# Kernel optimization log

Hardware: AMD Instinct MI355X
Metric: run time of the kernel (lower is better)

## Reference

```python
import math
import jax, jax.numpy as jnp
import numpy as np

N = 50000      # nodes
E = 800000     # edges
H = 128        # hidden_dim
NR = 16        # num_radial
CUTOFF = 5.0
LN_EPS = 1e-5


def _ln(h, g, b):
    m = jnp.mean(h, axis=-1, keepdims=True)
    v = jnp.mean((h - m) ** 2, axis=-1, keepdims=True)
    return (h - m) * jax.lax.rsqrt(v + LN_EPS) * g + b


def _legendre(angle):
    # degree=4 -> 4 polynomial features
    c = jnp.cos(angle)
    p0 = jnp.ones_like(c)
    p1 = c
    p2 = (3.0 * c * p1 - 1.0 * p0) / 2.0
    p3 = (5.0 * c * p2 - 2.0 * p1) / 3.0
    return jnp.concatenate([p0, p1, p2, p3], axis=-1)


def setup_inputs() -> dict:
    key = jax.random.key(0)
    ks = jax.random.split(key, 16)
    ED = 2 * H + NR + 3  # edge feature dim = 275

    def w(k, shape, fan_in):
        return jax.random.normal(k, shape, jnp.float32) / np.sqrt(fan_in).astype(np.float32)

    return {
        "x": jax.random.normal(ks[0], (N, H), jnp.float32),
        "pos": jax.random.normal(ks[1], (N, 3), jnp.float32),
        "charge": jax.random.normal(ks[2], (N, 1), jnp.float32),
        "edge_attr": jax.random.uniform(ks[3], (E, 4), jnp.float32),
        "edge_index": jax.random.randint(ks[4], (2, E), 0, N),
        "We1": w(ks[5], (ED, H), ED), "be1": jnp.zeros((H,), jnp.float32),
        "g1": jnp.ones((H,), jnp.float32), "bt1": jnp.zeros((H,), jnp.float32),
        "We2": w(ks[6], (H, H), H), "be2": jnp.zeros((H,), jnp.float32),
        "Wn": w(ks[7], (2 * H, H), 2 * H), "bn": jnp.zeros((H,), jnp.float32),
        "gn": jnp.ones((H,), jnp.float32), "btn": jnp.zeros((H,), jnp.float32),
        "Wc1": w(ks[8], (H, H // 2), H), "bc1": jnp.zeros((H // 2,), jnp.float32),
        "Wc2": w(ks[9], (H // 2, 1), H // 2), "bc2": jnp.zeros((1,), jnp.float32),
    }


def reference(x, pos, charge, edge_attr, edge_index,
              We1, be1, g1, bt1, We2, be2, Wn, bn, gn, btn,
              Wc1, bc1, Wc2, bc2):
    src, dst = edge_index[0], edge_index[1]

    rel = pos[dst] - pos[src]                                   # [E,3]
    dist = jnp.sqrt(jnp.sum(rel ** 2, axis=-1, keepdims=True) + 1e-8)
    unit = rel / jnp.clip(dist, 1e-6)

    # edge-attribute gate via Legendre basis of angle/dihedral
    af = _legendre(edge_attr[:, 0:1])
    df = _legendre(edge_attr[:, 1:2])
    a_score = jnp.mean(jnp.abs(af), axis=-1, keepdims=True) * edge_attr[:, 2:3]
    d_score = jnp.mean(jnp.abs(df), axis=-1, keepdims=True) * edge_attr[:, 3:4]
    gate = jnp.clip(1.0 + 0.6 * (a_score + d_score), 0.35, 2.5)  # [E,1]

    # spherical Bessel radial basis
    freq = jnp.arange(1, NR + 1, dtype=jnp.float32) * (math.pi / CUTOFF)
    clipped = jnp.clip(dist, 1e-6)
    rad = jnp.sin(freq * clipped) / clipped                      # [E,NR]

    qs, qd = charge[src], charge[dst]
    ef = jnp.concatenate([
        x[src], x[dst], rad * gate, dist / CUTOFF * gate,
        qs * qd * gate, jnp.abs(qs - qd) * gate], axis=-1)       # [E,275]

    h = jax.nn.silu(ef @ We1 + be1)
    h = _ln(h, g1, bt1)
    eh = jax.nn.silu(h @ We2 + be2)                              # [E,H]

    ones = jnp.ones((eh.shape[0], 1), eh.dtype)
    cnt = jnp.clip(jax.ops.segment_sum(ones, src, num_segments=N), 1.0)
    agg = jax.ops.segment_sum(eh, src, num_segments=N) / cnt     # scatter-mean

    coord = jax.nn.silu(eh @ Wc1 + bc1) @ Wc2 + bc2              # [E,1]
    delta = jax.ops.segment_sum(unit * coord * gate, src, num_segments=N) / cnt

    x_new = x + _ln(jax.nn.silu(jnp.concatenate([x, agg], axis=-1) @ Wn + bn), gn, btn)
    pos_new = pos + 0.1 * delta
    return (x_new, pos_new)
```

## Files before the change

### kernel.cpp

```cpp
#include <hip/hip_runtime.h>
#include <hip/hip_bf16.h>
#include <math.h>


#define HDIM 128
#define GN   16
#define TILE 64
#define HS   136
#define AUXS 32
#define NS   264

#define B_BE1 0
#define B_G1  128
#define B_BT1 256
#define B_BE2 384
#define B_BC1 512
#define B_WC2 576
#define B_BC2 640
#define B_BN  704
#define B_GN  832
#define B_BTN 960
#define BIAS_N 1088

typedef unsigned int uint32;
typedef float f32x4 __attribute__((ext_vector_type(4)));
typedef float f32x2 __attribute__((ext_vector_type(2)));
typedef short short8 __attribute__((ext_vector_type(8)));
typedef unsigned short u16x4 __attribute__((ext_vector_type(4)));

__device__ __forceinline__ float bf2f(__hip_bfloat16 h) { return __bfloat162float(h); }

template<bool BF> __device__ __forceinline__ f32x2 ld2(const void* p, size_t i) {
  if constexpr (BF) {
    uint32 u; __builtin_memcpy(&u, (const char*)p + i * 2, 4);
    f32x2 r; r.x = __uint_as_float(u << 16); r.y = __uint_as_float(u & 0xffff0000u);
    return r;
  } else {
    f32x2 r; __builtin_memcpy(&r, (const char*)p + i * 4, 8);
    return r;
  }
}
template<bool BF> __device__ __forceinline__ float ld1(const void* p, size_t i) {
  if constexpr (BF) {
    __hip_bfloat16 h; __builtin_memcpy(&h, (const char*)p + i * 2, 2);
    return bf2f(h);
  } else {
    float v; __builtin_memcpy(&v, (const char*)p + i * 4, 4);
    return v;
  }
}
template<bool BF> __device__ __forceinline__ void st1(void* p, size_t i, float v) {
  if constexpr (BF) {
    __hip_bfloat16 h = __float2bfloat16(v);
    __builtin_memcpy((char*)p + i * 2, &h, 2);
  } else {
    __builtin_memcpy((char*)p + i * 4, &v, 4);
  }
}

__device__ __forceinline__ unsigned short f2bf(float v) {
  __hip_bfloat16 h = __float2bfloat16(v);
  unsigned short u; __builtin_memcpy(&u, &h, 2);
  return u;
}

template<bool BF> __device__ __forceinline__ short8 ldxrow(const void* x, int row, int col) {
  if constexpr (BF) {
    return *reinterpret_cast<const short8*>((const char*)x + ((size_t)row * HDIM + col) * 2);
  } else {
    const float* p = (const float*)x + (size_t)row * HDIM + col;
    f32x4 v0 = *reinterpret_cast<const f32x4*>(p);
    f32x4 v1 = *reinterpret_cast<const f32x4*>(p + 4);
    short8 a;
    a[0] = (short)f2bf(v0.x); a[1] = (short)f2bf(v0.y);
    a[2] = (short)f2bf(v0.z); a[3] = (short)f2bf(v0.w);
    a[4] = (short)f2bf(v1.x); a[5] = (short)f2bf(v1.y);
    a[6] = (short)f2bf(v1.z); a[7] = (short)f2bf(v1.w);
    return a;
  }
}

__device__ __forceinline__ float silu(float v) { return v / (1.0f + __expf(-v)); }

__device__ __forceinline__ f32x4 splat4(float v) {
  f32x4 r; r.x = v; r.y = v; r.z = v; r.w = v; return r;
}

__device__ __forceinline__ void wave_sync() {
  asm volatile("s_waitcnt lgkmcnt(0)" ::: "memory");
}

__global__ void probe_kernel(const uint32* g1, int* flag) {
  if (threadIdx.x == 0 && blockIdx.x == 0) *flag = (g1[0] == 0x3F800000u) ? 0 : 1;
}

__global__ void hist_kernel(const int* __restrict__ ei, int* __restrict__ cnt, int E) {
  int e = blockIdx.x * 256 + threadIdx.x;
  if (e < E) atomicAdd(&cnt[ei[e]], 1);
}

__global__ void __launch_bounds__(1024) scan_kernel(const int* __restrict__ cnt,
                                                    int* __restrict__ off, int N) {
  __shared__ int part[16];
  __shared__ int carry_s;
  const int t = threadIdx.x;
  const int wid = t >> 6, ln = t & 63;
  if (t == 0) carry_s = 0;
  __syncthreads();
  for (int base = 0; base < N; base += 1024) {
    const int v = (base + t < N) ? cnt[base + t] : 0;
    int inc = v;
#pragma unroll
    for (int s = 1; s < 64; s <<= 1) {
      int u = __shfl_up(inc, s);
      if (ln >= s) inc += u;
    }
    if (ln == 63) part[wid] = inc;
    __syncthreads();
    if (wid == 0) {
      int p = (ln < 16) ? part[ln] : 0;
#pragma unroll
      for (int s = 1; s < 16; s <<= 1) {
        int u = __shfl_up(p, s);
        if (ln >= s) p += u;
      }
      if (ln < 16) part[ln] = p;
    }
    __syncthreads();
    const int woff = (wid > 0) ? part[wid - 1] : 0;
    const int carry = carry_s;
    if (base + t < N) off[base + t] = carry + inc + woff - v;
    __syncthreads();
    if (t == 1023) carry_s = carry + part[15];
    __syncthreads();
  }
  if (t == 0) off[N] = carry_s;
}

__global__ void fill_kernel(const int* __restrict__ ei, const int* __restrict__ off,
                            int* __restrict__ cursor, int* __restrict__ eidx, int E) {
  int e = blockIdx.x * 256 + threadIdx.x;
  if (e < E) {
    int s = ei[e];
    int p = atomicAdd(&cursor[s], 1);
    eidx[off[s] + p] = e;
  }
}

template<bool BF>
__global__ void __launch_bounds__(256) prep_kernel(
    const void* __restrict__ pos, const void* __restrict__ charge,
    const void* __restrict__ We1, const void* __restrict__ We2,
    const void* __restrict__ Wc1, const void* __restrict__ Wn,
    const void* __restrict__ be1, const void* __restrict__ g1,
    const void* __restrict__ bt1, const void* __restrict__ be2,
    const void* __restrict__ bc1, const void* __restrict__ wc2,
    const void* __restrict__ bc2, const void* __restrict__ bn,
    const void* __restrict__ gn, const void* __restrict__ btn,
    const int* __restrict__ flag,
    float* __restrict__ posf, float* __restrict__ chgf, float* __restrict__ biasf,
    __hip_bfloat16* __restrict__ WT1, __hip_bfloat16* __restrict__ WT2,
    __hip_bfloat16* __restrict__ WTc1, __hip_bfloat16* __restrict__ WTn,
    int N) {
  if (*flag != (BF ? 1 : 0)) return;
  const int gt = blockIdx.x * 256 + threadIdx.x;
  const int gs = gridDim.x * 256;
  for (int i = gt; i < N * 3; i += gs) posf[i] = ld1<BF>(pos, i);
  for (int i = gt; i < N; i += gs) chgf[i] = ld1<BF>(charge, i);
  for (int i = gt; i < 128; i += gs) {
    biasf[B_BE1 + i] = ld1<BF>(be1, i);
    biasf[B_G1  + i] = ld1<BF>(g1, i);
    biasf[B_BT1 + i] = ld1<BF>(bt1, i);
    biasf[B_BE2 + i] = ld1<BF>(be2, i);
    biasf[B_BN  + i] = ld1<BF>(bn, i);
    biasf[B_GN  + i] = ld1<BF>(gn, i);
    biasf[B_BTN + i] = ld1<BF>(btn, i);
  }
  for (int i = gt; i < 64; i += gs) {
    biasf[B_BC1 + i] = ld1<BF>(bc1, i);
    biasf[B_WC2 + i] = ld1<BF>(wc2, i);
  }
  if (gt == 0) biasf[B_BC2] = ld1<BF>(bc2, 0);
  for (int i = gt; i < 128 * 288; i += gs) {
    int n = i / 288, k = i % 288;
    float v = (k < 275) ? ld1<BF>(We1, (size_t)k * 128 + n) : 0.f;
    WT1[i] = __float2bfloat16(v);
  }
  for (int i = gt; i < 128 * 128; i += gs) {
    int n = i / 128, k = i % 128;
    WT2[i] = __float2bfloat16(ld1<BF>(We2, (size_t)k * 128 + n));
  }
  for (int i = gt; i < 64 * 128; i += gs) {
    int n = i / 128, k = i % 128;
    WTc1[i] = __float2bfloat16(ld1<BF>(Wc1, (size_t)k * 64 + n));
  }
  for (int i = gt; i < 128 * 256; i += gs) {
    int n = i / 256, k = i % 256;
    WTn[i] = __float2bfloat16(ld1<BF>(Wn, (size_t)k * 128 + n));
  }
}

template<bool BF>
__global__ void __launch_bounds__(256, 2) edge_mfma_kernel(
    const void* __restrict__ x, const void* __restrict__ eattr,
    const int* __restrict__ ei,
    const int* __restrict__ off, const int* __restrict__ eidx,
    const int* __restrict__ flag,
    const float* __restrict__ posf, const float* __restrict__ chgf,
    const float* __restrict__ biasf,
    const __hip_bfloat16* __restrict__ WT1, const __hip_bfloat16* __restrict__ WT2,
    const __hip_bfloat16* __restrict__ WTc1, const __hip_bfloat16* __restrict__ WTn,
    void* __restrict__ out, int N, int E) {
  if (*flag != (BF ? 1 : 0)) return;

  __shared__ __align__(16) __hip_bfloat16 hbuf[4 * 16 * HS];
  __shared__ __align__(16) __hip_bfloat16 aux_s[TILE * AUXS];
  __shared__ float base_s[GN * 132];
  __shared__ float agg_s[(GN + 1) * 132];
  __shared__ float dsum_s[(GN + 1) * 4];
  __shared__ float sgate[TILE];
  __shared__ float sunit[TILE * 3];
  __shared__ int sdst_s[TILE];
  __shared__ int offs[GN + 1];
  __shared__ short ssrc16[TILE];

  const int tid = threadIdx.x;
  const int w = tid >> 6;
  const int lane = tid & 63;
  const int g0 = blockIdx.x * GN;
  const int c16 = lane & 15;
  const int g4 = lane >> 4;

  for (int i = tid; i < (GN + 1) * 132; i += 256) agg_s[i] = 0.f;
  for (int i = tid; i < (GN + 1) * 4; i += 256) dsum_s[i] = 0.f;
  if (tid <= GN) {
    int node = g0 + tid;
    offs[tid] = off[node < N ? node : N];
  }
  __syncthreads();

  const int eStart = offs[0];
  const int eEnd = offs[GN];
  const int ntiles = (eEnd - eStart + TILE - 1) / TILE;

  __hip_bfloat16* hw = hbuf + (size_t)w * 16 * HS;

  const short* WT1s = reinterpret_cast<const short*>(WT1);
  const short* WT2s = reinterpret_cast<const short*>(WT2);
  const short* WTc1s = reinterpret_cast<const short*>(WTc1);

  {
    for (int i = tid; i < GN * 32; i += 256) {
      const int row = i >> 5, c4 = (i & 31) * 4;
      int node = g0 + row; node = (node < N) ? node : (N - 1);
      const size_t xb = (size_t)node * HDIM + c4;
      f32x2 v0 = ld2<BF>(x, xb);
      f32x2 v1 = ld2<BF>(x, xb + 2);
      u16x4 pk;
      pk[0] = f2bf(v0.x); pk[1] = f2bf(v0.y); pk[2] = f2bf(v1.x); pk[3] = f2bf(v1.y);
      *reinterpret_cast<u16x4*>(&hbuf[row * HS + c4]) = pk;
    }
    __syncthreads();
    f32x4 acc2[2];
#pragma unroll
    for (int j = 0; j < 2; j++)
      acc2[j] = splat4(biasf[B_BE1 + (2 * w + j) * 16 + c16]);
#pragma unroll
    for (int ks = 0; ks < 4; ks++) {
      short8 a = *reinterpret_cast<const short8*>(&hbuf[c16 * HS + ks * 32 + g4 * 8]);
#pragma unroll
      for (int j = 0; j < 2; j++) {
        const int nt = 2 * w + j;
        short8 b = *reinterpret_cast<const short8*>(
            &WT1s[(size_t)(nt * 16 + c16) * 288 + ks * 32 + g4 * 8]);
        acc2[j] = __builtin_amdgcn_mfma_f32_16x16x32_bf16(a, b, acc2[j], 0, 0, 0);
      }
    }
#pragma unroll
    for (int j = 0; j < 2; j++) {
      const int nt = 2 * w + j;
#pragma unroll
      for (int r = 0; r < 4; r++)
        base_s[(g4 * 4 + r) * 132 + nt * 16 + c16] = acc2[j][r];
    }
    __syncthreads();
  }

  const float FSC = 3.14159265358979323846f / 5.0f;

  for (int t = 0; t < ntiles; t++) {
    const int ebase = eStart + t * TILE + w * 16;

    {
      const int es = lane >> 2, sub = lane & 3, slot = w * 16 + es;
      const int pos_i = ebase + es;
      const bool valid = pos_i < eEnd;
      int loc = GN, dstn = g0;
      int eg = 0;
      if (valid) {
        loc = 0;
#pragma unroll
        for (int st = 8; st > 0; st >>= 1)
          if (loc + st <= GN - 1 && offs[loc + st] <= pos_i) loc += st;
        eg = eidx[pos_i];
        dstn = ei[(size_t)E + eg];
      }
      float gate = 0.f, dcl = 1.f, ux = 0.f, uy = 0.f, uz = 0.f;
      float f0 = 0.f, f1 = 0.f, f2 = 0.f;
      if (valid && sub == 0) {
        const int srcg = g0 + loc;
        const float px = posf[3 * srcg + 0], py = posf[3 * srcg + 1], pz = posf[3 * srcg + 2];
        const float qn = chgf[srcg];
        const float dx = posf[3 * dstn + 0] - px;
        const float dy = posf[3 * dstn + 1] - py;
        const float dz = posf[3 * dstn + 2] - pz;
        const float dist = sqrtf(dx * dx + dy * dy + dz * dz + 1e-8f);
        dcl = fmaxf(dist, 1e-6f);
        ux = dx / dcl; uy = dy / dcl; uz = dz / dcl;
        const float a_ = ld1<BF>(eattr, (size_t)eg * 4 + 0);
        const float dh = ld1<BF>(eattr, (size_t)eg * 4 + 1);
        const float w2a = ld1<BF>(eattr, (size_t)eg * 4 + 2);
        const float w3a = ld1<BF>(eattr, (size_t)eg * 4 + 3);
        const float ca = cosf(a_);
        const float p2a = 0.5f * (3.f * ca * ca - 1.f);
        const float p3a = (5.f * ca * p2a - 2.f * ca) * (1.f / 3.f);
        const float ma = 0.25f * (1.f + fabsf(ca) + fabsf(p2a) + fabsf(p3a));
        const float cd = cosf(dh);
        const float p2d = 0.5f * (3.f * cd * cd - 1.f);
        const float p3d = (5.f * cd * p2d - 2.f * cd) * (1.f / 3.f);
        const float md = 0.25f * (1.f + fabsf(cd) + fabsf(p2d) + fabsf(p3d));
        gate = fminf(fmaxf(1.f + 0.6f * (ma * w2a + md * w3a), 0.35f), 2.5f);
        const float qd = chgf[dstn];
        f0 = dist * 0.2f * gate;
        f1 = qn * qd * gate;
        f2 = fabsf(qn - qd) * gate;
      }
      const int bl = lane & ~3;
      dcl = __shfl(dcl, bl);
      gate = __shfl(gate, bl);
      u16x4 rv;
#pragma unroll
      for (int i = 0; i < 4; i++) {
        const float k1 = (float)(sub * 4 + i + 1);
        rv[i] = f2bf(sinf(FSC * k1 * dcl) / dcl * gate);
      }
      *reinterpret_cast<u16x4*>(&aux_s[slot * AUXS + sub * 4]) = rv;
      if (sub == 0) {
        sgate[slot] = gate;
        ssrc16[slot] = (short)loc;
        sdst_s[slot] = dstn;
        sunit[slot * 3 + 0] = ux; sunit[slot * 3 + 1] = uy;
        sunit[slot * 3 + 2] = uz;
        u16x4 ev;
        ev[0] = f2bf(f0); ev[1] = f2bf(f1); ev[2] = f2bf(f2); ev[3] = 0;
        *reinterpret_cast<u16x4*>(&aux_s[slot * AUXS + 16]) = ev;
      } else {
        u16x4 z; z[0] = 0; z[1] = 0; z[2] = 0; z[3] = 0;
        *reinterpret_cast<u16x4*>(&aux_s[slot * AUXS + 16 + sub * 4]) = z;
      }
    }
    wave_sync();

    int ssr[4];
#pragma unroll
    for (int r = 0; r < 4; r++) ssr[r] = (int)ssrc16[w * 16 + g4 * 4 + r];
    const int dstc = sdst_s[w * 16 + c16];

    f32x4 acc[8];
#pragma unroll
    for (int nt = 0; nt < 8; nt++) {
      f32x4 c;
#pragma unroll
      for (int r = 0; r < 4; r++) {
        const int sb = (ssr[r] < GN) ? ssr[r] : (GN - 1);
        c[r] = base_s[sb * 132 + nt * 16 + c16];
      }
      acc[nt] = c;
    }
#pragma unroll
    for (int ks = 0; ks < 4; ks++) {
      short8 a = ldxrow<BF>(x, dstc, ks * 32 + g4 * 8);
#pragma unroll
      for (int nt = 0; nt < 8; nt++) {
        short8 b = *reinterpret_cast<const short8*>(
            &WT1s[(size_t)(nt * 16 + c16) * 288 + 128 + ks * 32 + g4 * 8]);
        acc[nt] = __builtin_amdgcn_mfma_f32_16x16x32_bf16(a, b, acc[nt], 0, 0, 0);
      }
    }
    {
      short8 a = *reinterpret_cast<const short8*>(&aux_s[(w * 16 + c16) * AUXS + g4 * 8]);
#pragma unroll
      for (int nt = 0; nt < 8; nt++) {
        short8 b = *reinterpret_cast<const short8*>(
            &WT1s[(size_t)(nt * 16 + c16) * 288 + 256 + g4 * 8]);
        acc[nt] = __builtin_amdgcn_mfma_f32_16x16x32_bf16(a, b, acc[nt], 0, 0, 0);
      }
    }

    {
      float sm[4] = {0.f, 0.f, 0.f, 0.f}, sq[4] = {0.f, 0.f, 0.f, 0.f};
#pragma unroll
      for (int nt = 0; nt < 8; nt++)
#pragma unroll
        for (int r = 0; r < 4; r++) {
          const float v = silu(acc[nt][r]);
          acc[nt][r] = v;
          sm[r] += v;
          sq[r] += v * v;
        }
#pragma unroll
      for (int r = 0; r < 4; r++) {
#pragma unroll
        for (int mk = 1; mk <= 8; mk <<= 1) {
          sm[r] += __shfl_xor(sm[r], mk);
          sq[r] += __shfl_xor(sq[r], mk);
        }
      }
      float mu[4], rsd[4];
#pragma unroll
      for (int r = 0; r < 4; r++) {
        mu[r] = sm[r] * (1.f / HDIM);
        const float var = sq[r] * (1.f / HDIM) - mu[r] * mu[r];
        rsd[r] = rsqrtf(var + 1e-5f);
      }
#pragma unroll
      for (int nt = 0; nt < 8; nt++) {
        const float gg = biasf[B_G1 + nt * 16 + c16];
        const float bb = biasf[B_BT1 + nt * 16 + c16];
#pragma unroll
        for (int r = 0; r < 4; r++) {
          const int m = g4 * 4 + r;
          hw[m * HS + nt * 16 + c16] =
              __float2bfloat16((acc[nt][r] - mu[r]) * rsd[r] * gg + bb);
        }
      }
    }
    wave_sync();

#pragma unroll
    for (int nt = 0; nt < 8; nt++) acc[nt] = splat4(biasf[B_BE2 + nt * 16 + c16]);
#pragma unroll
    for (int ks = 0; ks < 4; ks++) {
      short8 a = *reinterpret_cast<const short8*>(&hw[c16 * HS + ks * 32 + g4 * 8]);
#pragma unroll
      for (int nt = 0; nt < 8; nt++) {
        short8 b = *reinterpret_cast<const short8*>(
            &WT2s[(size_t)(nt * 16 + c16) * 128 + ks * 32 + g4 * 8]);
        acc[nt] = __builtin_amdgcn_mfma_f32_16x16x32_bf16(a, b, acc[nt], 0, 0, 0);
      }
    }
#pragma unroll
    for (int nt = 0; nt < 8; nt++)
#pragma unroll
      for (int r = 0; r < 4; r++) {
        const float v = silu(acc[nt][r]);
        const int m = g4 * 4 + r;
        hw[m * HS + nt * 16 + c16] = __float2bfloat16(v);
        atomicAdd(&agg_s[ssr[r] * 132 + nt * 16 + c16], v);
      }
    wave_sync();

    {
      f32x4 a3[4];
#pragma unroll
      for (int q = 0; q < 4; q++) a3[q] = splat4(biasf[B_BC1 + q * 16 + c16]);
#pragma unroll
      for (int ks = 0; ks < 4; ks++) {
        short8 a = *reinterpret_cast<const short8*>(&hw[c16 * HS + ks * 32 + g4 * 8]);
#pragma unroll
        for (int q = 0; q < 4; q++) {
          short8 b = *reinterpret_cast<const short8*>(
              &WTc1s[(size_t)(q * 16 + c16) * 128 + ks * 32 + g4 * 8]);
          a3[q] = __builtin_amdgcn_mfma_f32_16x16x32_bf16(a, b, a3[q], 0, 0, 0);
        }
      }
      float cp[4] = {0.f, 0.f, 0.f, 0.f};
#pragma unroll
      for (int q = 0; q < 4; q++) {
        const float wv = biasf[B_WC2 + q * 16 + c16];
#pragma unroll
        for (int r = 0; r < 4; r++) cp[r] += silu(a3[q][r]) * wv;
      }
#pragma unroll
      for (int r = 0; r < 4; r++) {
#pragma unroll
        for (int mk = 1; mk <= 8; mk <<= 1) cp[r] += __shfl_xor(cp[r], mk);
      }
      const float bc2v = biasf[B_BC2];
      if (c16 < 4) {
        const int r = c16;
        const int slot = w * 16 + g4 * 4 + r;
        const float cr = (r == 0) ? cp[0] : (r == 1) ? cp[1] : (r == 2) ? cp[2] : cp[3];
        const float scale = (cr + bc2v) * sgate[slot];
        const int sl = (int)ssrc16[slot];
        atomicAdd(&dsum_s[sl * 4 + 0], sunit[slot * 3 + 0] * scale);
        atomicAdd(&dsum_s[sl * 4 + 1], sunit[slot * 3 + 1] * scale);
        atomicAdd(&dsum_s[sl * 4 + 2], sunit[slot * 3 + 2] * scale);
      }
    }
    wave_sync();
  }
  __syncthreads();

  if (w == 0) {
    for (int m = 0; m < GN; m++) {
      const int node = g0 + m;
      const bool nv = node < N;
      const int dg = nv ? (offs[m + 1] - offs[m]) : 0;
      const float inv = 1.f / fmaxf((float)dg, 1.f);
      const int cb = lane * 4;
      u16x4 pk;
#pragma unroll
      for (int j = 0; j < 4; j++) {
        const int col = cb + j;
        float v = 0.f;
        if (nv) {
          v = (col < 128) ? ld1<BF>(x, (size_t)node * HDIM + col)
                          : agg_s[m * 132 + (col - 128)] * inv;
        }
        pk[j] = f2bf(v);
      }
      *reinterpret_cast<u16x4*>(&hbuf[m * NS + cb]) = pk;
    }
    wave_sync();

    const short* WTns = reinterpret_cast<const short*>(WTn);
    f32x4 an[8];
#pragma unroll
    for (int nt = 0; nt < 8; nt++) an[nt] = splat4(biasf[B_BN + nt * 16 + c16]);
#pragma unroll
    for (int ks = 0; ks < 8; ks++) {
      short8 a = *reinterpret_cast<const short8*>(&hbuf[c16 * NS + ks * 32 + g4 * 8]);
#pragma unroll
      for (int nt = 0; nt < 8; nt++) {
        short8 b = *reinterpret_cast<const short8*>(
            &WTns[(size_t)(nt * 16 + c16) * 256 + ks * 32 + g4 * 8]);
        an[nt] = __builtin_amdgcn_mfma_f32_16x16x32_bf16(a, b, an[nt], 0, 0, 0);
      }
    }
    float sm[4] = {0.f, 0.f, 0.f, 0.f}, sq[4] = {0.f, 0.f, 0.f, 0.f};
#pragma unroll
    for (int nt = 0; nt < 8; nt++)
#pragma unroll
      for (int r = 0; r < 4; r++) {
        const float v = silu(an[nt][r]);
        an[nt][r] = v;
        sm[r] += v;
        sq[r] += v * v;
      }
#pragma unroll
    for (int r = 0; r < 4; r++) {
#pragma unroll
      for (int mk = 1; mk <= 8; mk <<= 1) {
        sm[r] += __shfl_xor(sm[r], mk);
        sq[r] += __shfl_xor(sq[r], mk);
      }
    }
    float mu[4], rsd[4];
#pragma unroll
    for (int r = 0; r < 4; r++) {
      mu[r] = sm[r] * (1.f / HDIM);
      const float var = sq[r] * (1.f / HDIM) - mu[r] * mu[r];
      rsd[r] = rsqrtf(var + 1e-5f);
    }
#pragma unroll
    for (int nt = 0; nt < 8; nt++) {
      const float gg = biasf[B_GN + nt * 16 + c16];
      const float bb = biasf[B_BTN + nt * 16 + c16];
#pragma unroll
      for (int r = 0; r < 4; r++) {
        const int m = g4 * 4 + r;
        const int node = g0 + m;
        if (node < N) {
          const int col = nt * 16 + c16;
          const float xo = ld1<BF>(x, (size_t)node * HDIM + col);
          st1<BF>(out, (size_t)node * HDIM + col,
                  xo + (an[nt][r] - mu[r]) * rsd[r] * gg + bb);
        }
      }
    }
    if (lane < GN) {
      const int node = g0 + lane;
      if (node < N) {
        const int dg = offs[lane + 1] - offs[lane];
        const float inv = 1.f / fmaxf((float)dg, 1.f);
#pragma unroll
        for (int d = 0; d < 3; d++) {
          const float pv = posf[(size_t)node * 3 + d] + 0.1f * dsum_s[lane * 4 + d] * inv;
          st1<BF>(out, (size_t)N * HDIM + (size_t)node * 3 + d, pv);
        }
      }
    }
  }
}

extern "C" void kernel_launch(void* const* d_in, const int* in_sizes, int n_in,
                              void* d_out, int out_size, void* d_ws, size_t ws_size,
                              hipStream_t stream) {
  const void* x      = d_in[0];
  const void* pos    = d_in[1];
  const void* charge = d_in[2];
  const void* eattr  = d_in[3];
  const int*  ei     = (const int*)d_in[4];
  const void* We1 = d_in[5];  const void* be1 = d_in[6];
  const void* g1  = d_in[7];  const void* bt1 = d_in[8];
  const void* We2 = d_in[9];  const void* be2 = d_in[10];
  const void* Wn  = d_in[11]; const void* bn  = d_in[12];
  const void* gn  = d_in[13]; const void* btn = d_in[14];
  const void* Wc1 = d_in[15]; const void* bc1 = d_in[16];
  const void* Wc2 = d_in[17]; const void* bc2 = d_in[18];

  const int N = in_sizes[0] / HDIM;
  const int E = in_sizes[3] / 4;

  int* wsI    = (int*)d_ws;
  int* flag   = wsI;
  int* cnt    = wsI + 1;
  int* cursor = cnt + N;
  int* off    = cursor + N;
  int* eidx   = off + (N + 1);

  char* base = (char*)d_ws;
  size_t o = ((size_t)(3 * N + 2 + E) * 4 + 511) & ~(size_t)511;
  float* posf = (float*)(base + o);
  o = (o + (size_t)N * 3 * 4 + 511) & ~(size_t)511;
  float* chgf = (float*)(base + o);
  o = (o + (size_t)N * 4 + 511) & ~(size_t)511;
  float* biasf = (float*)(base + o);
  o = (o + (size_t)BIAS_N * 4 + 511) & ~(size_t)511;
  __hip_bfloat16* WT1 = (__hip_bfloat16*)(base + o);
  o = (o + (size_t)128 * 288 * 2 + 511) & ~(size_t)511;
  __hip_bfloat16* WT2 = (__hip_bfloat16*)(base + o);
  o = (o + (size_t)128 * 128 * 2 + 511) & ~(size_t)511;
  __hip_bfloat16* WTc1 = (__hip_bfloat16*)(base + o);
  o = (o + (size_t)64 * 128 * 2 + 511) & ~(size_t)511;
  __hip_bfloat16* WTn = (__hip_bfloat16*)(base + o);

  hipMemsetAsync(d_ws, 0, (size_t)(1 + 2 * N) * sizeof(int), stream);

  probe_kernel<<<1, 64, 0, stream>>>((const uint32*)g1, flag);

  const int eb = (E + 255) / 256;
  hist_kernel<<<eb, 256, 0, stream>>>(ei, cnt, E);
  scan_kernel<<<1, 1024, 0, stream>>>(cnt, off, N);
  fill_kernel<<<eb, 256, 0, stream>>>(ei, off, cursor, eidx, E);

  prep_kernel<true><<<512, 256, 0, stream>>>(
      pos, charge, We1, We2, Wc1, Wn, be1, g1, bt1, be2, bc1, Wc2, bc2, bn, gn, btn,
      flag, posf, chgf, biasf, WT1, WT2, WTc1, WTn, N);
  prep_kernel<false><<<512, 256, 0, stream>>>(
      pos, charge, We1, We2, Wc1, Wn, be1, g1, bt1, be2, bc1, Wc2, bc2, bn, gn, btn,
      flag, posf, chgf, biasf, WT1, WT2, WTc1, WTn, N);

  const int nb = (N + GN - 1) / GN;
  edge_mfma_kernel<true><<<nb, 256, 0, stream>>>(
      x, eattr, ei, off, eidx, flag, posf, chgf, biasf, WT1, WT2, WTc1, WTn,
      d_out, N, E);
  edge_mfma_kernel<false><<<nb, 256, 0, stream>>>(
      x, eattr, ei, off, eidx, flag, posf, chgf, biasf, WT1, WT2, WTc1, WTn,
      d_out, N, E);
}
```

Baseline: 1.393 ms.

## Build edge geometry features in registers and prefetch next tile's edge indices

The per-edge geometry, gate and radial-basis features are now computed directly in the lanes that own each MFMA A-fragment row, instead of being staged through shared-memory aux buffers with wave syncs. The next tile's edge index and destination are loaded one iteration early to hide gather latency. The node-input packing before the node MLP is now spread across all four waves instead of one. In exchange, every lane in a 16-lane group redundantly computes the same geometry and gate, and register pressure rises.

Result: slower. 1.952 ms (+40.2%).

```diff
diff --git a/kernel.cpp b/kernel.cpp
--- a/kernel.cpp
+++ b/kernel.cpp
@@ -7,7 +7,6 @@
 #define GN   16
 #define TILE 64
 #define HS   136
-#define AUXS 32
 #define NS   264
 
 #define B_BE1 0
@@ -62,6 +61,21 @@
   __hip_bfloat16 h = __float2bfloat16(v);
   unsigned short u; __builtin_memcpy(&u, &h, 2);
   return u;
+}
+
+template<bool BF> __device__ __forceinline__ f32x4 ld4(const void* p, size_t i) {
+  if constexpr (BF) {
+    u16x4 u; __builtin_memcpy(&u, (const char*)p + i * 2, 8);
+    f32x4 r;
+    r.x = __uint_as_float((uint32)u[0] << 16);
+    r.y = __uint_as_float((uint32)u[1] << 16);
+    r.z = __uint_as_float((uint32)u[2] << 16);
+    r.w = __uint_as_float((uint32)u[3] << 16);
+    return r;
+  } else {
+    f32x4 r; __builtin_memcpy(&r, (const char*)p + i * 4, 16);
+    return r;
+  }
 }
 
 template<bool BF> __device__ __forceinline__ short8 ldxrow(const void* x, int row, int col) {
@@ -84,10 +98,6 @@
 
 __device__ __forceinline__ f32x4 splat4(float v) {
   f32x4 r; r.x = v; r.y = v; r.z = v; r.w = v; return r;
-}
-
-__device__ __forceinline__ void wave_sync() {
-  asm volatile("s_waitcnt lgkmcnt(0)" ::: "memory");
 }
 
 __global__ void probe_kernel(const uint32* g1, int* flag) {
@@ -214,15 +224,10 @@
   if (*flag != (BF ? 1 : 0)) return;
 
   __shared__ __align__(16) __hip_bfloat16 hbuf[4 * 16 * HS];
-  __shared__ __align__(16) __hip_bfloat16 aux_s[TILE * AUXS];
   __shared__ float base_s[GN * 132];
   __shared__ float agg_s[(GN + 1) * 132];
   __shared__ float dsum_s[(GN + 1) * 4];
-  __shared__ float sgate[TILE];
-  __shared__ float sunit[TILE * 3];
-  __shared__ int sdst_s[TILE];
   __shared__ int offs[GN + 1];
-  __shared__ short ssrc16[TILE];
 
   const int tid = threadIdx.x;
   const int w = tid >> 6;
@@ -288,83 +293,71 @@
 
   const float FSC = 3.14159265358979323846f / 5.0f;
 
+  int pos0 = eStart + w * 16 + c16;
+  bool vcur = (ntiles > 0) && (pos0 < eEnd);
+  int eg_cur = vcur ? eidx[pos0] : 0;
+  int dst_cur = vcur ? ei[(size_t)E + eg_cur] : g0;
+
   for (int t = 0; t < ntiles; t++) {
-    const int ebase = eStart + t * TILE + w * 16;
-
-    {
-      const int es = lane >> 2, sub = lane & 3, slot = w * 16 + es;
-      const int pos_i = ebase + es;
-      const bool valid = pos_i < eEnd;
-      int loc = GN, dstn = g0;
-      int eg = 0;
-      if (valid) {
-        loc = 0;
-#pragma unroll
-        for (int st = 8; st > 0; st >>= 1)
-          if (loc + st <= GN - 1 && offs[loc + st] <= pos_i) loc += st;
-        eg = eidx[pos_i];
-        dstn = ei[(size_t)E + eg];
-      }
-      float gate = 0.f, dcl = 1.f, ux = 0.f, uy = 0.f, uz = 0.f;
-      float f0 = 0.f, f1 = 0.f, f2 = 0.f;
-      if (valid && sub == 0) {
-        const int srcg = g0 + loc;
-        const float px = posf[3 * srcg + 0], py = posf[3 * srcg + 1], pz = posf[3 * srcg + 2];
-        const float qn = chgf[srcg];
-        const float dx = posf[3 * dstn + 0] - px;
-        const float dy = posf[3 * dstn + 1] - py;
-        const float dz = posf[3 * dstn + 2] - pz;
-        const float dist = sqrtf(dx * dx + dy * dy + dz * dz + 1e-8f);
-        dcl = fmaxf(dist, 1e-6f);
-        ux = dx / dcl; uy = dy / dcl; uz = dz / dcl;
-        const float a_ = ld1<BF>(eattr, (size_t)eg * 4 + 0);
-        const float dh = ld1<BF>(eattr, (size_t)eg * 4 + 1);
-        const float w2a = ld1<BF>(eattr, (size_t)eg * 4 + 2);
-        const float w3a = ld1<BF>(eattr, (size_t)eg * 4 + 3);
-        const float ca = cosf(a_);
-        const float p2a = 0.5f * (3.f * ca * ca - 1.f);
-        const float p3a = (5.f * ca * p2a - 2.f * ca) * (1.f / 3.f);
-        const float ma = 0.25f * (1.f + fabsf(ca) + fabsf(p2a) + fabsf(p3a));
-        const float cd = cosf(dh);
-        const float p2d = 0.5f * (3.f * cd * cd - 1.f);
-        const float p3d = (5.f * cd * p2d - 2.f * cd) * (1.f / 3.f);
-        const float md = 0.25f * (1.f + fabsf(cd) + fabsf(p2d) + fabsf(p3d));
-        gate = fminf(fmaxf(1.f + 0.6f * (ma * w2a + md * w3a), 0.35f), 2.5f);
-        const float qd = chgf[dstn];
-        f0 = dist * 0.2f * gate;
-        f1 = qn * qd * gate;
-        f2 = fabsf(qn - qd) * gate;
-      }
-      const int bl = lane & ~3;
-      dcl = __shfl(dcl, bl);
-      gate = __shfl(gate, bl);
-      u16x4 rv;
-#pragma unroll
-      for (int i = 0; i < 4; i++) {
-        const float k1 = (float)(sub * 4 + i + 1);
-        rv[i] = f2bf(sinf(FSC * k1 * dcl) / dcl * gate);
-      }
-      *reinterpret_cast<u16x4*>(&aux_s[slot * AUXS + sub * 4]) = rv;
-      if (sub == 0) {
-        sgate[slot] = gate;
-        ssrc16[slot] = (short)loc;
-        sdst_s[slot] = dstn;
-        sunit[slot * 3 + 0] = ux; sunit[slot * 3 + 1] = uy;
-        sunit[slot * 3 + 2] = uz;
-        u16x4 ev;
-        ev[0] = f2bf(f0); ev[1] = f2bf(f1); ev[2] = f2bf(f2); ev[3] = 0;
-        *reinterpret_cast<u16x4*>(&aux_s[slot * AUXS + 16]) = ev;
-      } else {
-        u16x4 z; z[0] = 0; z[1] = 0; z[2] = 0; z[3] = 0;
-        *reinterpret_cast<u16x4*>(&aux_s[slot * AUXS + 16 + sub * 4]) = z;
-      }
-    }
-    wave_sync();
+    const int pos_nx = eStart + (t + 1) * TILE + w * 16 + c16;
+    const bool v_nx = pos_nx < eEnd;
+    const int eg_nx = v_nx ? eidx[pos_nx] : 0;
+
+    const int pos_i = eStart + t * TILE + w * 16 + c16;
+    const bool valid = pos_i < eEnd;
+    int loc = 0;
+#pragma unroll
+    for (int st = 8; st > 0; st >>= 1)
+      if (loc + st <= GN - 1 && offs[loc + st] <= pos_i) loc += st;
+    int srcg = g0 + loc; srcg = (srcg < N) ? srcg : (N - 1);
+    const int dstn = dst_cur;
+
+    const float px = posf[3 * srcg + 0], py = posf[3 * srcg + 1], pz = posf[3 * srcg + 2];
+    const float qn = chgf[srcg];
+    const float dx = posf[3 * dstn + 0] - px;
+    const float dy = posf[3 * dstn + 1] - py;
+    const float dz = posf[3 * dstn + 2] - pz;
+    const float qd = chgf[dstn];
+    const float dist = sqrtf(dx * dx + dy * dy + dz * dz + 1e-8f);
+    const float dcl = fmaxf(dist, 1e-6f);
+    const float ux = dx / dcl, uy = dy / dcl, uz = dz / dcl;
+
+    f32x4 ea = splat4(0.f);
+    if (valid) ea = ld4<BF>(eattr, (size_t)eg_cur * 4);
+    const float ca = cosf(ea.x);
+    const float p2a = 0.5f * (3.f * ca * ca - 1.f);
+    const float p3a = (5.f * ca * p2a - 2.f * ca) * (1.f / 3.f);
+    const float ma = 0.25f * (1.f + fabsf(ca) + fabsf(p2a) + fabsf(p3a));
+    const float cd = cosf(ea.y);
+    const float p2d = 0.5f * (3.f * cd * cd - 1.f);
+    const float p3d = (5.f * cd * p2d - 2.f * cd) * (1.f / 3.f);
+    const float md = 0.25f * (1.f + fabsf(cd) + fabsf(p2d) + fabsf(p3d));
+    float gate = fminf(fmaxf(1.f + 0.6f * (ma * ea.z + md * ea.w), 0.35f), 2.5f);
+    gate = valid ? gate : 0.f;
+    const int locA = valid ? loc : GN;
+
+    short8 afrag;
+    if (g4 < 2) {
+#pragma unroll
+      for (int i = 0; i < 8; i++) {
+        const float k1 = (float)(g4 * 8 + i + 1);
+        afrag[i] = (short)f2bf(sinf(FSC * k1 * dcl) / dcl * gate);
+      }
+    } else if (g4 == 2) {
+      const float f0 = dist * 0.2f * gate;
+      const float f1 = qn * qd * gate;
+      const float f2 = fabsf(qn - qd) * gate;
+      afrag[0] = (short)f2bf(f0); afrag[1] = (short)f2bf(f1);
+      afrag[2] = (short)f2bf(f2); afrag[3] = 0;
+      afrag[4] = 0; afrag[5] = 0; afrag[6] = 0; afrag[7] = 0;
+    } else {
+#pragma unroll
+      for (int i = 0; i < 8; i++) afrag[i] = 0;
+    }
 
     int ssr[4];
 #pragma unroll
-    for (int r = 0; r < 4; r++) ssr[r] = (int)ssrc16[w * 16 + g4 * 4 + r];
-    const int dstc = sdst_s[w * 16 + c16];
+    for (int r = 0; r < 4; r++) ssr[r] = __shfl(locA, g4 * 4 + r);
 
     f32x4 acc[8];
 #pragma unroll
@@ -379,7 +372,7 @@
     }
 #pragma unroll
     for (int ks = 0; ks < 4; ks++) {
-      short8 a = ldxrow<BF>(x, dstc, ks * 32 + g4 * 8);
+      short8 a = ldxrow<BF>(x, dstn, ks * 32 + g4 * 8);
 #pragma unroll
       for (int nt = 0; nt < 8; nt++) {
         short8 b = *reinterpret_cast<const short8*>(
@@ -387,14 +380,11 @@
         acc[nt] = __builtin_amdgcn_mfma_f32_16x16x32_bf16(a, b, acc[nt], 0, 0, 0);
       }
     }
-    {
-      short8 a = *reinterpret_cast<const short8*>(&aux_s[(w * 16 + c16) * AUXS + g4 * 8]);
-#pragma unroll
-      for (int nt = 0; nt < 8; nt++) {
-        short8 b = *reinterpret_cast<const short8*>(
-            &WT1s[(size_t)(nt * 16 + c16) * 288 + 256 + g4 * 8]);
-        acc[nt] = __builtin_amdgcn_mfma_f32_16x16x32_bf16(a, b, acc[nt], 0, 0, 0);
-      }
+#pragma unroll
+    for (int nt = 0; nt < 8; nt++) {
+      short8 b = *reinterpret_cast<const short8*>(
+          &WT1s[(size_t)(nt * 16 + c16) * 288 + 256 + g4 * 8]);
+      acc[nt] = __builtin_amdgcn_mfma_f32_16x16x32_bf16(afrag, b, acc[nt], 0, 0, 0);
     }
 
     {
@@ -435,7 +425,6 @@
         }
       }
     }
-    wave_sync();
 
 #pragma unroll
     for (int nt = 0; nt < 8; nt++) acc[nt] = splat4(biasf[B_BE2 + nt * 16 + c16]);
@@ -458,7 +447,6 @@
         hw[m * HS + nt * 16 + c16] = __float2bfloat16(v);
         atomicAdd(&agg_s[ssr[r] * 132 + nt * 16 + c16], v);
       }
-    wave_sync();
 
     {
       f32x4 a3[4];
@@ -486,44 +474,51 @@
 #pragma unroll
         for (int mk = 1; mk <= 8; mk <<= 1) cp[r] += __shfl_xor(cp[r], mk);
       }
+      const int esrc = g4 * 4 + (c16 & 3);
+      const float uxs = __shfl(ux, esrc);
+      const float uys = __shfl(uy, esrc);
+      const float uzs = __shfl(uz, esrc);
+      const float gts = __shfl(gate, esrc);
+      const int locs = __shfl(locA, esrc);
       const float bc2v = biasf[B_BC2];
       if (c16 < 4) {
         const int r = c16;
-        const int slot = w * 16 + g4 * 4 + r;
         const float cr = (r == 0) ? cp[0] : (r == 1) ? cp[1] : (r == 2) ? cp[2] : cp[3];
-        const float scale = (cr + bc2v) * sgate[slot];
-        const int sl = (int)ssrc16[slot];
-        atomicAdd(&dsum_s[sl * 4 + 0], sunit[slot * 3 + 0] * scale);
-        atomicAdd(&dsum_s[sl * 4 + 1], sunit[slot * 3 + 1] * scale);
-        atomicAdd(&dsum_s[sl * 4 + 2], sunit[slot * 3 + 2] * scale);
-      }
-    }
-    wave_sync();
+        const float scale = (cr + bc2v) * gts;
+        atomicAdd(&dsum_s[locs * 4 + 0], uxs * scale);
+        atomicAdd(&dsum_s[locs * 4 + 1], uys * scale);
+        atomicAdd(&dsum_s[locs * 4 + 2], uzs * scale);
+      }
+    }
+
+    const int dst_nx = v_nx ? ei[(size_t)E + eg_nx] : g0;
+    eg_cur = eg_nx;
+    dst_cur = dst_nx;
   }
   __syncthreads();
 
+  for (int m = w; m < GN; m += 4) {
+    const int node = g0 + m;
+    const bool nv = node < N;
+    const int dg = nv ? (offs[m + 1] - offs[m]) : 0;
+    const float inv = 1.f / fmaxf((float)dg, 1.f);
+    const int cb = lane * 4;
+    u16x4 pk;
+#pragma unroll
+    for (int j = 0; j < 4; j++) {
+      const int col = cb + j;
+      float v = 0.f;
+      if (nv) {
+        v = (col < 128) ? ld1<BF>(x, (size_t)node * HDIM + col)
+                        : agg_s[m * 132 + (col - 128)] * inv;
+      }
+      pk[j] = f2bf(v);
+    }
+    *reinterpret_cast<u16x4*>(&hbuf[m * NS + cb]) = pk;
+  }
+  __syncthreads();
+
   if (w == 0) {
-    for (int m = 0; m < GN; m++) {
-      const int node = g0 + m;
-      const bool nv = node < N;
-      const int dg = nv ? (offs[m + 1] - offs[m]) : 0;
-      const float inv = 1.f / fmaxf((float)dg, 1.f);
-      const int cb = lane * 4;
-      u16x4 pk;
-#pragma unroll
-      for (int j = 0; j < 4; j++) {
-        const int col = cb + j;
-        float v = 0.f;
-        if (nv) {
-          v = (col < 128) ? ld1<BF>(x, (size_t)node * HDIM + col)
-                          : agg_s[m * 132 + (col - 128)] * inv;
-        }
-        pk[j] = f2bf(v);
-      }
-      *reinterpret_cast<u16x4*>(&hbuf[m * NS + cb]) = pk;
-    }
-    wave_sync();
-
     const short* WTns = reinterpret_cast<const short*>(WTn);
     f32x4 an[8];
 #pragma unroll
```

## Pre-convert x to bf16, prefetch next edge indices, parallelize node epilogue staging

Applied to the files above, without the earlier changes.

In the fp32 path, the prep kernel converts x to bf16 once into workspace, and the edge kernel then gathers bf16 rows for x[dst] instead of loading fp32 and converting per edge. That halves gather bytes on the dominant random-access load. It also software-prefetches the next tile's edge id and destination index, and loads edge_attr as a single vector. The node-update staging is spread across all four waves instead of one. The cost is an extra pass over x and dependence on workspace size, with a fallback path if it does not fit.

Measured after the change: 1.310 ms. 1.06x faster.

```diff
diff --git a/kernel.cpp b/kernel.cpp
--- a/kernel.cpp
+++ b/kernel.cpp
@@ -62,6 +62,21 @@
   __hip_bfloat16 h = __float2bfloat16(v);
   unsigned short u; __builtin_memcpy(&u, &h, 2);
   return u;
+}
+
+template<bool BF> __device__ __forceinline__ f32x4 ld4(const void* p, size_t i) {
+  if constexpr (BF) {
+    u16x4 u; __builtin_memcpy(&u, (const char*)p + i * 2, 8);
+    f32x4 r;
+    r.x = __uint_as_float((uint32)u[0] << 16);
+    r.y = __uint_as_float((uint32)u[1] << 16);
+    r.z = __uint_as_float((uint32)u[2] << 16);
+    r.w = __uint_as_float((uint32)u[3] << 16);
+    return r;
+  } else {
+    f32x4 r; __builtin_memcpy(&r, (const char*)p + i * 4, 16);
+    return r;
+  }
 }
 
 template<bool BF> __device__ __forceinline__ short8 ldxrow(const void* x, int row, int col) {
@@ -149,6 +164,7 @@
 
 template<bool BF>
 __global__ void __launch_bounds__(256) prep_kernel(
+    const void* __restrict__ x,
     const void* __restrict__ pos, const void* __restrict__ charge,
     const void* __restrict__ We1, const void* __restrict__ We2,
     const void* __restrict__ Wc1, const void* __restrict__ Wn,
@@ -161,12 +177,16 @@
     float* __restrict__ posf, float* __restrict__ chgf, float* __restrict__ biasf,
     __hip_bfloat16* __restrict__ WT1, __hip_bfloat16* __restrict__ WT2,
     __hip_bfloat16* __restrict__ WTc1, __hip_bfloat16* __restrict__ WTn,
+    __hip_bfloat16* __restrict__ xbf,
     int N) {
   if (*flag != (BF ? 1 : 0)) return;
   const int gt = blockIdx.x * 256 + threadIdx.x;
   const int gs = gridDim.x * 256;
   for (int i = gt; i < N * 3; i += gs) posf[i] = ld1<BF>(pos, i);
   for (int i = gt; i < N; i += gs) chgf[i] = ld1<BF>(charge, i);
+  if (xbf) {
+    for (int i = gt; i < N * HDIM; i += gs) xbf[i] = __float2bfloat16(ld1<BF>(x, i));
+  }
   for (int i = gt; i < 128; i += gs) {
     biasf[B_BE1 + i] = ld1<BF>(be1, i);
     biasf[B_G1  + i] = ld1<BF>(g1, i);
@@ -200,7 +220,7 @@
   }
 }
 
-template<bool BF>
+template<bool BF, bool XB>
 __global__ void __launch_bounds__(256, 2) edge_mfma_kernel(
     const void* __restrict__ x, const void* __restrict__ eattr,
     const int* __restrict__ ei,
@@ -210,6 +230,7 @@
     const float* __restrict__ biasf,
     const __hip_bfloat16* __restrict__ WT1, const __hip_bfloat16* __restrict__ WT2,
     const __hip_bfloat16* __restrict__ WTc1, const __hip_bfloat16* __restrict__ WTn,
+    const __hip_bfloat16* __restrict__ xbf,
     void* __restrict__ out, int N, int E) {
   if (*flag != (BF ? 1 : 0)) return;
 
@@ -248,17 +269,23 @@
   const short* WT1s = reinterpret_cast<const short*>(WT1);
   const short* WT2s = reinterpret_cast<const short*>(WT2);
   const short* WTc1s = reinterpret_cast<const short*>(WTc1);
+  const short* xbs = reinterpret_cast<const short*>(xbf);
 
   {
     for (int i = tid; i < GN * 32; i += 256) {
       const int row = i >> 5, c4 = (i & 31) * 4;
       int node = g0 + row; node = (node < N) ? node : (N - 1);
-      const size_t xb = (size_t)node * HDIM + c4;
-      f32x2 v0 = ld2<BF>(x, xb);
-      f32x2 v1 = ld2<BF>(x, xb + 2);
-      u16x4 pk;
-      pk[0] = f2bf(v0.x); pk[1] = f2bf(v0.y); pk[2] = f2bf(v1.x); pk[3] = f2bf(v1.y);
-      *reinterpret_cast<u16x4*>(&hbuf[row * HS + c4]) = pk;
+      if constexpr (XB) {
+        *reinterpret_cast<u16x4*>(&hbuf[row * HS + c4]) =
+            *reinterpret_cast<const u16x4*>(&xbs[(size_t)node * HDIM + c4]);
+      } else {
+        const size_t xb = (size_t)node * HDIM + c4;
+        f32x2 v0 = ld2<BF>(x, xb);
+        f32x2 v1 = ld2<BF>(x, xb + 2);
+        u16x4 pk;
+        pk[0] = f2bf(v0.x); pk[1] = f2bf(v0.y); pk[2] = f2bf(v1.x); pk[3] = f2bf(v1.y);
+        *reinterpret_cast<u16x4*>(&hbuf[row * HS + c4]) = pk;
+      }
     }
     __syncthreads();
     f32x4 acc2[2];
@@ -288,23 +315,28 @@
 
   const float FSC = 3.14159265358979323846f / 5.0f;
 
+  const int es_pl = lane >> 2;
+  int pos_cur = eStart + w * 16 + es_pl;
+  bool v_cur = (ntiles > 0) && (pos_cur < eEnd);
+  int eg_cur = v_cur ? eidx[pos_cur] : 0;
+  int dst_cur = v_cur ? ei[(size_t)E + eg_cur] : g0;
+
   for (int t = 0; t < ntiles; t++) {
-    const int ebase = eStart + t * TILE + w * 16;
+    const int pos_nx = pos_cur + TILE;
+    const bool v_nx = pos_nx < eEnd;
+    const int eg_nx = v_nx ? eidx[pos_nx] : 0;
 
     {
-      const int es = lane >> 2, sub = lane & 3, slot = w * 16 + es;
-      const int pos_i = ebase + es;
-      const bool valid = pos_i < eEnd;
-      int loc = GN, dstn = g0;
-      int eg = 0;
+      const int es = es_pl, sub = lane & 3, slot = w * 16 + es;
+      const bool valid = v_cur;
+      int loc = GN;
       if (valid) {
         loc = 0;
 #pragma unroll
         for (int st = 8; st > 0; st >>= 1)
-          if (loc + st <= GN - 1 && offs[loc + st] <= pos_i) loc += st;
-        eg = eidx[pos_i];
-        dstn = ei[(size_t)E + eg];
-      }
+          if (loc + st <= GN - 1 && offs[loc + st] <= pos_cur) loc += st;
+      }
+      const int dstn = dst_cur;
       float gate = 0.f, dcl = 1.f, ux = 0.f, uy = 0.f, uz = 0.f;
       float f0 = 0.f, f1 = 0.f, f2 = 0.f;
       if (valid && sub == 0) {
@@ -317,19 +349,16 @@
         const float dist = sqrtf(dx * dx + dy * dy + dz * dz + 1e-8f);
         dcl = fmaxf(dist, 1e-6f);
         ux = dx / dcl; uy = dy / dcl; uz = dz / dcl;
-        const float a_ = ld1<BF>(eattr, (size_t)eg * 4 + 0);
-        const float dh = ld1<BF>(eattr, (size_t)eg * 4 + 1);
-        const float w2a = ld1<BF>(eattr, (size_t)eg * 4 + 2);
-        const float w3a = ld1<BF>(eattr, (size_t)eg * 4 + 3);
-        const float ca = cosf(a_);
+        f32x4 ea = ld4<BF>(eattr, (size_t)eg_cur * 4);
+        const float ca = cosf(ea.x);
         const float p2a = 0.5f * (3.f * ca * ca - 1.f);
         const float p3a = (5.f * ca * p2a - 2.f * ca) * (1.f / 3.f);
         const float ma = 0.25f * (1.f + fabsf(ca) + fabsf(p2a) + fabsf(p3a));
-        const float cd = cosf(dh);
+        const float cd = cosf(ea.y);
         const float p2d = 0.5f * (3.f * cd * cd - 1.f);
         const float p3d = (5.f * cd * p2d - 2.f * cd) * (1.f / 3.f);
         const float md = 0.25f * (1.f + fabsf(cd) + fabsf(p2d) + fabsf(p3d));
-        gate = fminf(fmaxf(1.f + 0.6f * (ma * w2a + md * w3a), 0.35f), 2.5f);
+        gate = fminf(fmaxf(1.f + 0.6f * (ma * ea.z + md * ea.w), 0.35f), 2.5f);
         const float qd = chgf[dstn];
         f0 = dist * 0.2f * gate;
         f1 = qn * qd * gate;
@@ -347,7 +376,7 @@
       *reinterpret_cast<u16x4*>(&aux_s[slot * AUXS + sub * 4]) = rv;
       if (sub == 0) {
         sgate[slot] = gate;
-        ssrc16[slot] = (short)loc;
+        ssrc16[slot] = (short)(valid ? loc : GN);
         sdst_s[slot] = dstn;
         sunit[slot * 3 + 0] = ux; sunit[slot * 3 + 1] = uy;
         sunit[slot * 3 + 2] = uz;
@@ -379,7 +408,13 @@
     }
 #pragma unroll
     for (int ks = 0; ks < 4; ks++) {
-      short8 a = ldxrow<BF>(x, dstc, ks * 32 + g4 * 8);
+      short8 a;
+      if constexpr (XB) {
+        a = *reinterpret_cast<const short8*>(
+            &xbs[(size_t)dstc * HDIM + ks * 32 + g4 * 8]);
+      } else {
+        a = ldxrow<BF>(x, dstc, ks * 32 + g4 * 8);
+      }
 #pragma unroll
       for (int nt = 0; nt < 8; nt++) {
         short8 b = *reinterpret_cast<const short8*>(
@@ -499,31 +534,43 @@
       }
     }
     wave_sync();
+
+    const int dst_nx = v_nx ? ei[(size_t)E + eg_nx] : g0;
+    pos_cur = pos_nx;
+    v_cur = v_nx;
+    eg_cur = eg_nx;
+    dst_cur = dst_nx;
   }
   __syncthreads();
 
-  if (w == 0) {
-    for (int m = 0; m < GN; m++) {
-      const int node = g0 + m;
-      const bool nv = node < N;
-      const int dg = nv ? (offs[m + 1] - offs[m]) : 0;
-      const float inv = 1.f / fmaxf((float)dg, 1.f);
-      const int cb = lane * 4;
-      u16x4 pk;
+  for (int m = w; m < GN; m += 4) {
+    const int node = g0 + m;
+    const bool nv = node < N;
+    const int dg = nv ? (offs[m + 1] - offs[m]) : 0;
+    const float inv = 1.f / fmaxf((float)dg, 1.f);
+    const int cb = lane * 4;
+    u16x4 pk;
+    if (nv && cb < 128) {
+      if constexpr (XB) {
+        pk = *reinterpret_cast<const u16x4*>(&xbs[(size_t)node * HDIM + cb]);
+      } else {
+#pragma unroll
+        for (int j = 0; j < 4; j++) pk[j] = f2bf(ld1<BF>(x, (size_t)node * HDIM + cb + j));
+      }
+    } else {
 #pragma unroll
       for (int j = 0; j < 4; j++) {
         const int col = cb + j;
         float v = 0.f;
-        if (nv) {
-          v = (col < 128) ? ld1<BF>(x, (size_t)node * HDIM + col)
-                          : agg_s[m * 132 + (col - 128)] * inv;
-        }
+        if (nv && col >= 128) v = agg_s[m * 132 + (col - 128)] * inv;
         pk[j] = f2bf(v);
       }
-      *reinterpret_cast<u16x4*>(&hbuf[m * NS + cb]) = pk;
-    }
-    wave_sync();
-
+    }
+    *reinterpret_cast<u16x4*>(&hbuf[m * NS + cb]) = pk;
+  }
+  __syncthreads();
+
+  if (w == 0) {
     const short* WTns = reinterpret_cast<const short*>(WTn);
     f32x4 an[8];
 #pragma unroll
@@ -635,6 +682,9 @@
   __hip_bfloat16* WTc1 = (__hip_bfloat16*)(base + o);
   o = (o + (size_t)64 * 128 * 2 + 511) & ~(size_t)511;
   __hip_bfloat16* WTn = (__hip_bfloat16*)(base + o);
+  o = (o + (size_t)128 * 256 * 2 + 511) & ~(size_t)511;
+  __hip_bfloat16* xbf_ws = (__hip_bfloat16*)(base + o);
+  const bool xb_fits = (o + (size_t)N * HDIM * 2) <= ws_size;
 
   hipMemsetAsync(d_ws, 0, (size_t)(1 + 2 * N) * sizeof(int), stream);
 
@@ -646,17 +696,23 @@
   fill_kernel<<<eb, 256, 0, stream>>>(ei, off, cursor, eidx, E);
 
   prep_kernel<true><<<512, 256, 0, stream>>>(
-      pos, charge, We1, We2, Wc1, Wn, be1, g1, bt1, be2, bc1, Wc2, bc2, bn, gn, btn,
-      flag, posf, chgf, biasf, WT1, WT2, WTc1, WTn, N);
+      x, pos, charge, We1, We2, Wc1, Wn, be1, g1, bt1, be2, bc1, Wc2, bc2, bn, gn, btn,
+      flag, posf, chgf, biasf, WT1, WT2, WTc1, WTn, nullptr, N);
   prep_kernel<false><<<512, 256, 0, stream>>>(
-      pos, charge, We1, We2, Wc1, Wn, be1, g1, bt1, be2, bc1, Wc2, bc2, bn, gn, btn,
-      flag, posf, chgf, biasf, WT1, WT2, WTc1, WTn, N);
+      x, pos, charge, We1, We2, Wc1, Wn, be1, g1, bt1, be2, bc1, Wc2, bc2, bn, gn, btn,
+      flag, posf, chgf, biasf, WT1, WT2, WTc1, WTn, xb_fits ? xbf_ws : nullptr, N);
 
   const int nb = (N + GN - 1) / GN;
-  edge_mfma_kernel<true><<<nb, 256, 0, stream>>>(
+  edge_mfma_kernel<true, true><<<nb, 256, 0, stream>>>(
       x, eattr, ei, off, eidx, flag, posf, chgf, biasf, WT1, WT2, WTc1, WTn,
-      d_out, N, E);
-  edge_mfma_kernel<false><<<nb, 256, 0, stream>>>(
-      x, eattr, ei, off, eidx, flag, posf, chgf, biasf, WT1, WT2, WTc1, WTn,
-      d_out, N, E);
-}
+      (const __hip_bfloat16*)x, d_out, N, E);
+  if (xb_fits) {
+    edge_mfma_kernel<false, true><<<nb, 256, 0, stream>>>(
+        x, eattr, ei, off, eidx, flag, posf, chgf, biasf, WT1, WT2, WTc1, WTn,
+        xbf_ws, d_out, N, E);
+  } else {
+    edge_mfma_kernel<false, false><<<nb, 256, 0, stream>>>(
+        x, eattr, ei, off, eidx, flag, posf, chgf, biasf, WT1, WT2, WTc1, WTn,
+        nullptr, d_out, N, E);
+  }
+}
```
